# Kernel tuning notes

Hardware: AMD Instinct MI355X
Metric: run time of the kernel (lower is better)

## Reference

```python
import jax, jax.numpy as jnp
import numpy as np

NEG_BIG = -9e15
ALPHA = 0.2  # LeakyReLU negative slope


def setup_inputs() -> dict:
    key = jax.random.key(0)
    k1, k2, k3, k4 = jax.random.split(key, 4)
    N, Fin, Fout = 8192, 256, 256
    input_ = jax.random.normal(k1, (N, Fin), dtype=jnp.float32)
    adj = jax.random.randint(k2, (N, N), 0, 2, dtype=jnp.int32)
    # xavier_uniform with gain=1.414
    limW = 1.414 * np.sqrt(6.0 / (Fin + Fout))
    W = jax.random.uniform(k3, (Fin, Fout), minval=-limW, maxval=limW, dtype=jnp.float32)
    lima = 1.414 * np.sqrt(6.0 / (2 * Fout + 1))
    a = jax.random.uniform(k4, (2 * Fout, 1), minval=-lima, maxval=lima, dtype=jnp.float32)
    return {"input_": input_, "adj": adj, "W": W, "a": a}


def reference(input_, adj, W, a):
    # h: [N, F]
    h = input_ @ W
    F = h.shape[1]
    # Decompose cat([h_i, h_j]) @ a into per-node projections summed by broadcast
    src = h @ a[:F, 0]   # [N]  contribution of row node i
    dst = h @ a[F:, 0]   # [N]  contribution of col node j
    e = jax.nn.leaky_relu(src[:, None] + dst[None, :], negative_slope=ALPHA)  # [N, N]
    e = jnp.where(adj > 0, e, NEG_BIG)
    attention = jax.nn.softmax(e, axis=1)
    h_prime = attention @ h  # [N, F]
    return jax.nn.relu(h_prime)  # concat=True
```

## Files before the change

### kernel.cpp

```cpp
#include <hip/hip_runtime.h>
#include <math.h>

#define NN 8192
#define FF 256
#define ALPHA 0.2f
#define SS 4
#define JSEG (NN / SS)
#define STEPS (JSEG / 32)

typedef __bf16 bf16x8 __attribute__((ext_vector_type(8)));
typedef __bf16 bf16x4 __attribute__((ext_vector_type(4)));
typedef float  f32x4  __attribute__((ext_vector_type(4)));

__device__ __forceinline__ void dma16(const void* g, void* l) {
    __builtin_amdgcn_global_load_lds((const __attribute__((address_space(1))) void*)g,
                                     (__attribute__((address_space(3))) void*)l,
                                     16, 0, 0);
}

#define VMCNT0   asm volatile("s_waitcnt vmcnt(0)" ::: "memory")
#define LGKM0    asm volatile("s_waitcnt lgkmcnt(0)" ::: "memory")
#define BARRIER  asm volatile("s_barrier" ::: "memory")
#define FENCE    asm volatile("" ::: "memory")

__global__ __launch_bounds__(256) void k0_wt(const float* __restrict__ W,
                                             __bf16* __restrict__ WT) {
    __shared__ float ts[64][65];
    const int t = threadIdx.x;
    const int k0 = blockIdx.x * 64;
    const int n0 = blockIdx.y * 64;
    #pragma unroll
    for (int r = 0; r < 4; ++r) {
        int krow = r * 16 + (t >> 4);
        int nc4 = (t & 15) * 4;
        *(float4*)&ts[krow][nc4] = *(const float4*)&W[(size_t)(k0 + krow) * FF + n0 + nc4];
    }
    __syncthreads();
    const int nloc = t >> 2;
    const int kc = (t & 3) * 16;
    union { bf16x8 v[2]; __bf16 e[16]; } hi, lo;
    #pragma unroll
    for (int u = 0; u < 16; ++u) {
        float x = ts[kc + u][nloc];
        __bf16 h1 = (__bf16)x;
        hi.e[u] = h1;
        lo.e[u] = (__bf16)(x - (float)h1);
    }
    size_t base = (size_t)(n0 + nloc) * FF + k0 + kc;
    *(bf16x8*)&WT[base] = hi.v[0];
    *(bf16x8*)&WT[base + 8] = hi.v[1];
    size_t lbase = (size_t)FF * FF + base;
    *(bf16x8*)&WT[lbase] = lo.v[0];
    *(bf16x8*)&WT[lbase + 8] = lo.v[1];
}

__global__ __launch_bounds__(256) void k1_h(const float* __restrict__ X,
                                            const __bf16* __restrict__ WT,
                                            const float* __restrict__ a,
                                            __bf16* __restrict__ hT,
                                            float* __restrict__ src,
                                            float* __restrict__ dst) {
    __shared__ __bf16 ax[2][32][40];
    __shared__ float hs[32][264];
    __shared__ float red[2][4][32];
    const int t = threadIdx.x;
    const int i0 = blockIdx.x * 32;
    const int l = t & 63, wv = t >> 6, ln = l & 15, g = l >> 4;
    f32x4 acc[2][4];
    #pragma unroll
    for (int mt = 0; mt < 2; ++mt)
        #pragma unroll
        for (int nt = 0; nt < 4; ++nt)
            acc[mt][nt] = (f32x4){0.f, 0.f, 0.f, 0.f};

    for (int ks = 0; ks < 8; ++ks) {
        const int k0 = ks * 32;
        {
            int row = t >> 3, c4 = (t & 7) * 4;
            float4 xv = *(const float4*)&X[(size_t)(i0 + row) * FF + k0 + c4];
            bf16x4 hi4, lo4;
            float xs_[4] = {xv.x, xv.y, xv.z, xv.w};
            #pragma unroll
            for (int u = 0; u < 4; ++u) {
                __bf16 h1 = (__bf16)xs_[u];
                hi4[u] = h1;
                lo4[u] = (__bf16)(xs_[u] - (float)h1);
            }
            *(bf16x4*)&ax[0][row][c4] = hi4;
            *(bf16x4*)&ax[1][row][c4] = lo4;
        }
        __syncthreads();
        bf16x8 ah[2], al[2];
        ah[0] = *(bf16x8*)&ax[0][ln][g * 8];
        ah[1] = *(bf16x8*)&ax[0][16 + ln][g * 8];
        al[0] = *(bf16x8*)&ax[1][ln][g * 8];
        al[1] = *(bf16x8*)&ax[1][16 + ln][g * 8];
        #pragma unroll
        for (int nt = 0; nt < 4; ++nt) {
            const int n = wv * 64 + nt * 16 + ln;
            bf16x8 bh8 = *(const bf16x8*)&WT[(size_t)n * FF + k0 + g * 8];
            bf16x8 bl8 = *(const bf16x8*)&WT[(size_t)(FF + n) * FF + k0 + g * 8];
            #pragma unroll
            for (int mt = 0; mt < 2; ++mt) {
                acc[mt][nt] = __builtin_amdgcn_mfma_f32_16x16x32_bf16(ah[mt], bh8, acc[mt][nt], 0, 0, 0);
                acc[mt][nt] = __builtin_amdgcn_mfma_f32_16x16x32_bf16(ah[mt], bl8, acc[mt][nt], 0, 0, 0);
                acc[mt][nt] = __builtin_amdgcn_mfma_f32_16x16x32_bf16(al[mt], bh8, acc[mt][nt], 0, 0, 0);
            }
        }
        __syncthreads();
    }
    float an[4], ad[4];
    #pragma unroll
    for (int nt = 0; nt < 4; ++nt) {
        an[nt] = a[wv * 64 + nt * 16 + ln];
        ad[nt] = a[FF + wv * 64 + nt * 16 + ln];
    }
    float sp[2][4], dp[2][4];
    #pragma unroll
    for (int mt = 0; mt < 2; ++mt)
        #pragma unroll
        for (int rg = 0; rg < 4; ++rg) { sp[mt][rg] = 0.f; dp[mt][rg] = 0.f; }
    #pragma unroll
    for (int mt = 0; mt < 2; ++mt)
        #pragma unroll
        for (int nt = 0; nt < 4; ++nt)
            #pragma unroll
            for (int rg = 0; rg < 4; ++rg) {
                float v = acc[mt][nt][rg];
                hs[mt * 16 + g * 4 + rg][wv * 64 + nt * 16 + ln] = v;
                sp[mt][rg] += v * an[nt];
                dp[mt][rg] += v * ad[nt];
            }
    #pragma unroll
    for (int mk = 1; mk < 16; mk <<= 1)
        #pragma unroll
        for (int mt = 0; mt < 2; ++mt)
            #pragma unroll
            for (int rg = 0; rg < 4; ++rg) {
                sp[mt][rg] += __shfl_xor(sp[mt][rg], mk);
                dp[mt][rg] += __shfl_xor(dp[mt][rg], mk);
            }
    if (ln == 0) {
        #pragma unroll
        for (int mt = 0; mt < 2; ++mt)
            #pragma unroll
            for (int rg = 0; rg < 4; ++rg) {
                red[0][wv][mt * 16 + g * 4 + rg] = sp[mt][rg];
                red[1][wv][mt * 16 + g * 4 + rg] = dp[mt][rg];
            }
    }
    __syncthreads();
    if (t < 32) {
        src[i0 + t] = red[0][0][t] + red[0][1][t] + red[0][2][t] + red[0][3][t];
        dst[i0 + t] = red[1][0][t] + red[1][1][t] + red[1][2][t] + red[1][3][t];
    }
    {
        const int f = t;
        #pragma unroll
        for (int jc = 0; jc < 4; ++jc) {
            union { bf16x8 v; __bf16 e[8]; } hi;
            #pragma unroll
            for (int u = 0; u < 8; ++u) {
                float x = hs[jc * 8 + u][f];
                hi.e[u] = (__bf16)x;
            }
            *(bf16x8*)&hT[(size_t)f * NN + i0 + jc * 8] = hi.v;
        }
    }
}

__global__ __launch_bounds__(256) void k2a_pack(const int* __restrict__ adj,
                                                unsigned* __restrict__ bits) {
    const size_t total4 = (size_t)NN * NN / 4;
    const int l = threadIdx.x & 63;
    const int base = l & 56;
    size_t t = (size_t)blockIdx.x * 256 + threadIdx.x;
    const size_t stride = (size_t)gridDim.x * 256;
    for (; t < total4; t += stride) {
        int4 v = ((const int4*)adj)[t];
        unsigned nib = (unsigned)(v.x > 0) | ((unsigned)(v.y > 0) << 1)
                     | ((unsigned)(v.z > 0) << 2) | ((unsigned)(v.w > 0) << 3);
        unsigned w = 0;
        #pragma unroll
        for (int k = 0; k < 8; ++k)
            w |= (unsigned)__shfl((int)nib, base + k) << (4 * k);
        if ((l & 7) == 0)
            bits[t >> 3] = w;
    }
}

__global__ __launch_bounds__(256) void k2b_max(const float* __restrict__ dst,
                                               float* __restrict__ maxd) {
    __shared__ float red[256];
    float m = -1e30f;
    #pragma unroll
    for (int r = 0; r < NN / 1024; ++r) {
        float4 v = *(const float4*)&dst[(r * 256 + threadIdx.x) * 4];
        m = fmaxf(m, fmaxf(fmaxf(v.x, v.y), fmaxf(v.z, v.w)));
    }
    red[threadIdx.x] = m;
    __syncthreads();
    for (int s = 128; s > 0; s >>= 1) {
        if (threadIdx.x < s) red[threadIdx.x] = fmaxf(red[threadIdx.x], red[threadIdx.x + s]);
        __syncthreads();
    }
    if (threadIdx.x == 0) maxd[0] = red[0];
}

__global__ __launch_bounds__(256, 3) void k3_attn(const unsigned* __restrict__ bits,
                                                  const __bf16* __restrict__ hT,
                                                  const float* __restrict__ src,
                                                  const float* __restrict__ dst,
                                                  const float* __restrict__ maxd,
                                                  float* __restrict__ num,
                                                  float* __restrict__ den) {
    __shared__ __bf16 bh[2][1024 * 8];
    __shared__ unsigned mlds[64 * 68];
    __shared__ float dsts[JSEG];
    const int t = threadIdx.x;
    const int l = t & 63, wv = t >> 6, ln = l & 15, g = l >> 4;
    const int it = blockIdx.x & 127;
    const int seg = blockIdx.x >> 7;
    const int i0 = it * 64;
    const int jbeg = seg * JSEG;
    const int rl = wv * 16 + ln;
    const int row = i0 + rl;
    const float maxdv = maxd[0];
    const float src_r = src[row];
    const float e0 = src_r + maxdv;
    const float m_r = e0 > 0.f ? e0 : ALPHA * e0;

    {
        int r = t >> 2;
        const int4* gsrc = (const int4*)(bits + (size_t)(i0 + r) * (NN / 32) + (jbeg >> 5));
        int4* ldst = (int4*)&mlds[r * 68];
        #pragma unroll
        for (int u = 0; u < 4; ++u)
            ldst[u * 4 + (t & 3)] = gsrc[u * 4 + (t & 3)];
    }
    #pragma unroll
    for (int u = 0; u < 2; ++u)
        *(float4*)&dsts[(u * 256 + t) * 4] = *(const float4*)&dst[jbeg + (u * 256 + t) * 4];

    int ga[4], cb[4];
    #pragma unroll
    for (int r = 0; r < 4; ++r) {
        int cbase = r * 256 + wv * 64;
        int c = cbase + l;
        int f = c >> 2;
        int pc = c & 3;
        int jc = pc ^ ((f >> 1) & 3);
        ga[r] = f * NN + jc * 8;
        cb[r] = __builtin_amdgcn_readfirstlane(cbase);
    }
    const int rb = ln * 64 + ((g ^ ((ln >> 1) & 3)) * 16);
    const char* bh0 = (const char*)&bh[0][0] + rb;
    const char* bh1 = (const char*)&bh[1][0] + rb;

    #pragma unroll
    for (int r = 0; r < 4; ++r)
        dma16(&hT[ga[r] + jbeg], &bh[0][cb[r] * 8]);
    __syncthreads();

    float den_reg = 0.f;
    f32x4 acc[16];
    #pragma unroll
    for (int nt = 0; nt < 16; ++nt) acc[nt] = (f32x4){0.f, 0.f, 0.f, 0.f};

    for (int s = 0; s < STEPS; ++s) {
        unsigned mb = (mlds[rl * 68 + s] >> (g * 8)) & 0xffu;
        const float* dp = &dsts[s * 32 + g * 8];
        float4 dq0 = *(const float4*)dp;
        float4 dq1 = *(const float4*)(dp + 4);
        const float dv[8] = {dq0.x, dq0.y, dq0.z, dq0.w,
                             dq1.x, dq1.y, dq1.z, dq1.w};
        union { bf16x8 v; __bf16 e[8]; } af;
        #pragma unroll
        for (int u = 0; u < 8; ++u) {
            float e = src_r + dv[u];
            e = e > 0.f ? e : ALPHA * e;
            float ex = __expf(e - m_r);
            float w = (mb & (1u << u)) ? ex : 0.f;
            den_reg += w;
            af.e[u] = (__bf16)w;
        }
        FENCE; VMCNT0; LGKM0; BARRIER;
        {
            int sn = (s + 1 < STEPS) ? s + 1 : 0;
            int jn = jbeg + sn * 32;
            int p = (s + 1) & 1;
            #pragma unroll
            for (int r = 0; r < 4; ++r)
                dma16(&hT[ga[r] + jn], &bh[p][cb[r] * 8]);
        }
        FENCE;
        const char* bp = (s & 1) ? bh1 : bh0;
        #pragma unroll
        for (int nt = 0; nt < 16; ++nt) {
            bf16x8 bfr = *(const bf16x8*)(bp + nt * 1024);
            acc[nt] = __builtin_amdgcn_mfma_f32_16x16x32_bf16(af.v, bfr, acc[nt], 0, 0, 0);
        }
    }
    den_reg += __shfl_xor(den_reg, 16);
    den_reg += __shfl_xor(den_reg, 32);
    if (g == 0) den[(size_t)seg * NN + row] = den_reg;
    #pragma unroll
    for (int nt = 0; nt < 16; ++nt)
        #pragma unroll
        for (int rg = 0; rg < 4; ++rg)
            num[((size_t)seg * NN + i0 + wv * 16 + g * 4 + rg) * FF
                + nt * 16 + ln] = acc[nt][rg];
}

__global__ __launch_bounds__(256) void k4_out(const float* __restrict__ num,
                                              const float* __restrict__ den,
                                              float* __restrict__ out) {
    size_t f4 = (size_t)blockIdx.x * 256 + threadIdx.x;
    int i = (int)(f4 >> 6);
    int c4 = (int)(f4 & 63) << 2;
    float4 s = make_float4(0.f, 0.f, 0.f, 0.f);
    float d = 0.f;
    #pragma unroll
    for (int sg = 0; sg < SS; ++sg) {
        float4 v = *(const float4*)&num[((size_t)sg * NN + i) * FF + c4];
        s.x += v.x; s.y += v.y; s.z += v.z; s.w += v.w;
        d += den[(size_t)sg * NN + i];
    }
    float inv = 1.f / d;
    float4 o;
    o.x = fmaxf(s.x * inv, 0.f);
    o.y = fmaxf(s.y * inv, 0.f);
    o.z = fmaxf(s.z * inv, 0.f);
    o.w = fmaxf(s.w * inv, 0.f);
    *(float4*)&out[(size_t)i * FF + c4] = o;
}

extern "C" void kernel_launch(void* const* d_in, const int* in_sizes, int n_in,
                              void* d_out, int out_size, void* d_ws, size_t ws_size,
                              hipStream_t stream) {
    const float* X  = (const float*)d_in[0];
    const int*  adj = (const int*)d_in[1];
    const float* W  = (const float*)d_in[2];
    const float* a  = (const float*)d_in[3];
    float* out = (float*)d_out;
    char* ws = (char*)d_ws;

    const size_t off_hT   = 0;
    const size_t off_wt   = off_hT + (size_t)FF * NN * 2;
    const size_t off_src  = off_wt + (size_t)2 * FF * FF * 2;
    const size_t off_dst  = off_src + (size_t)NN * 4;
    const size_t off_maxd = off_dst + (size_t)NN * 4;
    const size_t off_num  = off_maxd + 256;
    const size_t off_den  = off_num + (size_t)SS * NN * FF * 4;
    const size_t off_bits = off_den + (size_t)SS * NN * 4;

    __bf16* hT_ws = (__bf16*)(ws + off_hT);
    __bf16* wt_ws = (__bf16*)(ws + off_wt);
    float* src_ws = (float*)(ws + off_src);
    float* dst_ws = (float*)(ws + off_dst);
    float* maxd   = (float*)(ws + off_maxd);
    float* num_ws = (float*)(ws + off_num);
    float* den_ws = (float*)(ws + off_den);
    unsigned* bits_ws = (unsigned*)(ws + off_bits);

    k2a_pack<<<2048, 256, 0, stream>>>(adj, bits_ws);
    k0_wt<<<dim3(FF / 64, FF / 64), 256, 0, stream>>>(W, wt_ws);
    k1_h<<<NN / 32, 256, 0, stream>>>(X, wt_ws, a, hT_ws, src_ws, dst_ws);
    k2b_max<<<1, 256, 0, stream>>>(dst_ws, maxd);
    k3_attn<<<(NN / 64) * SS, 256, 0, stream>>>(bits_ws, hT_ws, src_ws, dst_ws, maxd,
                                                num_ws, den_ws);
    k4_out<<<(NN * FF / 4) / 256, 256, 0, stream>>>(num_ws, den_ws, out);
}
```

Before: 456.2 us.

## Fuse adjacency bit-packing into attention kernel and triple-buffer hT DMA

Removes the separate adjacency packing kernel; each attention block now reads its int32 adjacency tile directly and packs it into LDS bitmasks via wave shuffles. The hT tile pipeline moves from double to triple buffering with a partial vmcnt wait so one DMA stays in flight across the barrier. This avoids a launch and the bits round-trip, but raises LDS use, drops occupancy target to 2 blocks per CU, and puts the adjacency load latency in the kernel prologue.

```diff
diff --git a/kernel.cpp b/kernel.cpp
--- a/kernel.cpp
+++ b/kernel.cpp
@@ -18,7 +18,7 @@
                                      16, 0, 0);
 }
 
-#define VMCNT0   asm volatile("s_waitcnt vmcnt(0)" ::: "memory")
+#define VMCNT4   asm volatile("s_waitcnt vmcnt(4)" ::: "memory")
 #define LGKM0    asm volatile("s_waitcnt lgkmcnt(0)" ::: "memory")
 #define BARRIER  asm volatile("s_barrier" ::: "memory")
 #define FENCE    asm volatile("" ::: "memory")
@@ -169,26 +169,6 @@
     }
 }
 
-__global__ __launch_bounds__(256) void k2a_pack(const int* __restrict__ adj,
-                                                unsigned* __restrict__ bits) {
-    const size_t total4 = (size_t)NN * NN / 4;
-    const int l = threadIdx.x & 63;
-    const int base = l & 56;
-    size_t t = (size_t)blockIdx.x * 256 + threadIdx.x;
-    const size_t stride = (size_t)gridDim.x * 256;
-    for (; t < total4; t += stride) {
-        int4 v = ((const int4*)adj)[t];
-        unsigned nib = (unsigned)(v.x > 0) | ((unsigned)(v.y > 0) << 1)
-                     | ((unsigned)(v.z > 0) << 2) | ((unsigned)(v.w > 0) << 3);
-        unsigned w = 0;
-        #pragma unroll
-        for (int k = 0; k < 8; ++k)
-            w |= (unsigned)__shfl((int)nib, base + k) << (4 * k);
-        if ((l & 7) == 0)
-            bits[t >> 3] = w;
-    }
-}
-
 __global__ __launch_bounds__(256) void k2b_max(const float* __restrict__ dst,
                                                float* __restrict__ maxd) {
     __shared__ float red[256];
@@ -207,14 +187,14 @@
     if (threadIdx.x == 0) maxd[0] = red[0];
 }
 
-__global__ __launch_bounds__(256, 3) void k3_attn(const unsigned* __restrict__ bits,
+__global__ __launch_bounds__(256, 2) void k3_attn(const int* __restrict__ adj,
                                                   const __bf16* __restrict__ hT,
                                                   const float* __restrict__ src,
                                                   const float* __restrict__ dst,
                                                   const float* __restrict__ maxd,
                                                   float* __restrict__ num,
                                                   float* __restrict__ den) {
-    __shared__ __bf16 bh[2][1024 * 8];
+    __shared__ __bf16 bh[3][1024 * 8];
     __shared__ unsigned mlds[64 * 68];
     __shared__ float dsts[JSEG];
     const int t = threadIdx.x;
@@ -230,18 +210,6 @@
     const float e0 = src_r + maxdv;
     const float m_r = e0 > 0.f ? e0 : ALPHA * e0;
 
-    {
-        int r = t >> 2;
-        const int4* gsrc = (const int4*)(bits + (size_t)(i0 + r) * (NN / 32) + (jbeg >> 5));
-        int4* ldst = (int4*)&mlds[r * 68];
-        #pragma unroll
-        for (int u = 0; u < 4; ++u)
-            ldst[u * 4 + (t & 3)] = gsrc[u * 4 + (t & 3)];
-    }
-    #pragma unroll
-    for (int u = 0; u < 2; ++u)
-        *(float4*)&dsts[(u * 256 + t) * 4] = *(const float4*)&dst[jbeg + (u * 256 + t) * 4];
-
     int ga[4], cb[4];
     #pragma unroll
     for (int r = 0; r < 4; ++r) {
@@ -254,19 +222,44 @@
         cb[r] = __builtin_amdgcn_readfirstlane(cbase);
     }
     const int rb = ln * 64 + ((g ^ ((ln >> 1) & 3)) * 16);
-    const char* bh0 = (const char*)&bh[0][0] + rb;
-    const char* bh1 = (const char*)&bh[1][0] + rb;
 
     #pragma unroll
     for (int r = 0; r < 4; ++r)
         dma16(&hT[ga[r] + jbeg], &bh[0][cb[r] * 8]);
+    FENCE;
+
+    {
+        const int sh = 4 * (t & 7);
+        #pragma unroll 4
+        for (int itp = 0; itp < 128; ++itp) {
+            int r = itp >> 1, p = itp & 1;
+            int4 v = *(const int4*)&adj[(size_t)(i0 + r) * NN + jbeg + p * 1024 + 4 * t];
+            unsigned x = ((unsigned)(v.x > 0) | ((unsigned)(v.y > 0) << 1)
+                        | ((unsigned)(v.z > 0) << 2) | ((unsigned)(v.w > 0) << 3)) << sh;
+            x |= __shfl_xor((int)x, 1);
+            x |= __shfl_xor((int)x, 2);
+            x |= __shfl_xor((int)x, 4);
+            if ((l & 7) == 0)
+                mlds[r * 68 + p * 32 + (t >> 3)] = x;
+        }
+    }
+    #pragma unroll
+    for (int u = 0; u < 2; ++u)
+        *(float4*)&dsts[(u * 256 + t) * 4] = *(const float4*)&dst[jbeg + (u * 256 + t) * 4];
+
     __syncthreads();
+
+    #pragma unroll
+    for (int r = 0; r < 4; ++r)
+        dma16(&hT[ga[r] + jbeg + 32], &bh[1][cb[r] * 8]);
+    FENCE;
 
     float den_reg = 0.f;
     f32x4 acc[16];
     #pragma unroll
     for (int nt = 0; nt < 16; ++nt) acc[nt] = (f32x4){0.f, 0.f, 0.f, 0.f};
 
+    int cur = 0;
     for (int s = 0; s < STEPS; ++s) {
         unsigned mb = (mlds[rl * 68 + s] >> (g * 8)) & 0xffu;
         const float* dp = &dsts[s * 32 + g * 8];
@@ -284,22 +277,25 @@
             den_reg += w;
             af.e[u] = (__bf16)w;
         }
-        FENCE; VMCNT0; LGKM0; BARRIER;
+        FENCE; VMCNT4; LGKM0; BARRIER;
         {
-            int sn = (s + 1 < STEPS) ? s + 1 : 0;
+            int sn = s + 2;
+            if (sn >= STEPS) sn -= STEPS;
             int jn = jbeg + sn * 32;
-            int p = (s + 1) & 1;
+            int dmb = cur + 2;
+            if (dmb >= 3) dmb -= 3;
             #pragma unroll
             for (int r = 0; r < 4; ++r)
-                dma16(&hT[ga[r] + jn], &bh[p][cb[r] * 8]);
+                dma16(&hT[ga[r] + jn], &bh[dmb][cb[r] * 8]);
         }
         FENCE;
-        const char* bp = (s & 1) ? bh1 : bh0;
+        const char* bp = (const char*)&bh[cur][0] + rb;
         #pragma unroll
         for (int nt = 0; nt < 16; ++nt) {
             bf16x8 bfr = *(const bf16x8*)(bp + nt * 1024);
             acc[nt] = __builtin_amdgcn_mfma_f32_16x16x32_bf16(af.v, bfr, acc[nt], 0, 0, 0);
         }
+        if (++cur == 3) cur = 0;
     }
     den_reg += __shfl_xor(den_reg, 16);
     den_reg += __shfl_xor(den_reg, 32);
@@ -352,7 +348,6 @@
     const size_t off_maxd = off_dst + (size_t)NN * 4;
     const size_t off_num  = off_maxd + 256;
     const size_t off_den  = off_num + (size_t)SS * NN * FF * 4;
-    const size_t off_bits = off_den + (size_t)SS * NN * 4;
 
     __bf16* hT_ws = (__bf16*)(ws + off_hT);
     __bf16* wt_ws = (__bf16*)(ws + off_wt);
@@ -361,13 +356,11 @@
     float* maxd   = (float*)(ws + off_maxd);
     float* num_ws = (float*)(ws + off_num);
     float* den_ws = (float*)(ws + off_den);
-    unsigned* bits_ws = (unsigned*)(ws + off_bits);
-
-    k2a_pack<<<2048, 256, 0, stream>>>(adj, bits_ws);
+
     k0_wt<<<dim3(FF / 64, FF / 64), 256, 0, stream>>>(W, wt_ws);
     k1_h<<<NN / 32, 256, 0, stream>>>(X, wt_ws, a, hT_ws, src_ws, dst_ws);
     k2b_max<<<1, 256, 0, stream>>>(dst_ws, maxd);
-    k3_attn<<<(NN / 64) * SS, 256, 0, stream>>>(bits_ws, hT_ws, src_ws, dst_ws, maxd,
+    k3_attn<<<(NN / 64) * SS, 256, 0, stream>>>(adj, hT_ws, src_ws, dst_ws, maxd,
                                                 num_ws, den_ws);
     k4_out<<<(NN * FF / 4) / 256, 256, 0, stream>>>(num_ws, den_ws, out);
 }
```

New measurement: 472.4 us. 3.6% more time.

## Replace LDS DMA with register-staged prefetch two steps ahead in attention kernel

Applied to the files above, without the earlier changes.

The attention kernel no longer uses global_load_lds DMA with an explicit vmcnt wait and barrier every step. It now loads hT tiles into registers two steps ahead, writes them into the alternate LDS buffer between MFMA phases, and unrolls the loop by two with one __syncthreads per half-step. Occupancy hint drops from 3 to 2 blocks per SIMD to make room for the extra staging registers. The aim is to hide global latency behind the weight computation and MFMAs, at the cost of more VGPRs, lower occupancy and explicit LDS stores.

```diff
diff --git a/kernel.cpp b/kernel.cpp
--- a/kernel.cpp
+++ b/kernel.cpp
@@ -11,17 +11,6 @@
 typedef __bf16 bf16x8 __attribute__((ext_vector_type(8)));
 typedef __bf16 bf16x4 __attribute__((ext_vector_type(4)));
 typedef float  f32x4  __attribute__((ext_vector_type(4)));
-
-__device__ __forceinline__ void dma16(const void* g, void* l) {
-    __builtin_amdgcn_global_load_lds((const __attribute__((address_space(1))) void*)g,
-                                     (__attribute__((address_space(3))) void*)l,
-                                     16, 0, 0);
-}
-
-#define VMCNT0   asm volatile("s_waitcnt vmcnt(0)" ::: "memory")
-#define LGKM0    asm volatile("s_waitcnt lgkmcnt(0)" ::: "memory")
-#define BARRIER  asm volatile("s_barrier" ::: "memory")
-#define FENCE    asm volatile("" ::: "memory")
 
 __global__ __launch_bounds__(256) void k0_wt(const float* __restrict__ W,
                                              __bf16* __restrict__ WT) {
@@ -207,7 +196,7 @@
     if (threadIdx.x == 0) maxd[0] = red[0];
 }
 
-__global__ __launch_bounds__(256, 3) void k3_attn(const unsigned* __restrict__ bits,
+__global__ __launch_bounds__(256, 2) void k3_attn(const unsigned* __restrict__ bits,
                                                   const __bf16* __restrict__ hT,
                                                   const float* __restrict__ src,
                                                   const float* __restrict__ dst,
@@ -230,6 +219,25 @@
     const float e0 = src_r + maxdv;
     const float m_r = e0 > 0.f ? e0 : ALPHA * e0;
 
+    int ga[4], lc[4];
+    #pragma unroll
+    for (int r = 0; r < 4; ++r) {
+        int c = r * 256 + wv * 64 + l;
+        int f = c >> 2;
+        int pc = c & 3;
+        int jc = pc ^ ((f >> 1) & 3);
+        ga[r] = f * NN + jc * 8;
+        lc[r] = c * 8;
+    }
+    const int rb = ln * 64 + ((g ^ ((ln >> 1) & 3)) * 16);
+    const char* bh0 = (const char*)&bh[0][0] + rb;
+    const char* bh1 = (const char*)&bh[1][0] + rb;
+
+    int4 rA[4], rB[4];
+    #pragma unroll
+    for (int r = 0; r < 4; ++r) rA[r] = *(const int4*)&hT[ga[r] + jbeg];
+    #pragma unroll
+    for (int r = 0; r < 4; ++r) rB[r] = *(const int4*)&hT[ga[r] + jbeg + 32];
     {
         int r = t >> 2;
         const int4* gsrc = (const int4*)(bits + (size_t)(i0 + r) * (NN / 32) + (jbeg >> 5));
@@ -241,25 +249,8 @@
     #pragma unroll
     for (int u = 0; u < 2; ++u)
         *(float4*)&dsts[(u * 256 + t) * 4] = *(const float4*)&dst[jbeg + (u * 256 + t) * 4];
-
-    int ga[4], cb[4];
-    #pragma unroll
-    for (int r = 0; r < 4; ++r) {
-        int cbase = r * 256 + wv * 64;
-        int c = cbase + l;
-        int f = c >> 2;
-        int pc = c & 3;
-        int jc = pc ^ ((f >> 1) & 3);
-        ga[r] = f * NN + jc * 8;
-        cb[r] = __builtin_amdgcn_readfirstlane(cbase);
-    }
-    const int rb = ln * 64 + ((g ^ ((ln >> 1) & 3)) * 16);
-    const char* bh0 = (const char*)&bh[0][0] + rb;
-    const char* bh1 = (const char*)&bh[1][0] + rb;
-
-    #pragma unroll
-    for (int r = 0; r < 4; ++r)
-        dma16(&hT[ga[r] + jbeg], &bh[0][cb[r] * 8]);
+    #pragma unroll
+    for (int r = 0; r < 4; ++r) *(int4*)&bh[0][lc[r]] = rA[r];
     __syncthreads();
 
     float den_reg = 0.f;
@@ -267,39 +258,60 @@
     #pragma unroll
     for (int nt = 0; nt < 16; ++nt) acc[nt] = (f32x4){0.f, 0.f, 0.f, 0.f};
 
-    for (int s = 0; s < STEPS; ++s) {
-        unsigned mb = (mlds[rl * 68 + s] >> (g * 8)) & 0xffu;
-        const float* dp = &dsts[s * 32 + g * 8];
-        float4 dq0 = *(const float4*)dp;
-        float4 dq1 = *(const float4*)(dp + 4);
-        const float dv[8] = {dq0.x, dq0.y, dq0.z, dq0.w,
-                             dq1.x, dq1.y, dq1.z, dq1.w};
-        union { bf16x8 v; __bf16 e[8]; } af;
-        #pragma unroll
-        for (int u = 0; u < 8; ++u) {
-            float e = src_r + dv[u];
-            e = e > 0.f ? e : ALPHA * e;
-            float ex = __expf(e - m_r);
-            float w = (mb & (1u << u)) ? ex : 0.f;
-            den_reg += w;
-            af.e[u] = (__bf16)w;
-        }
-        FENCE; VMCNT0; LGKM0; BARRIER;
-        {
-            int sn = (s + 1 < STEPS) ? s + 1 : 0;
-            int jn = jbeg + sn * 32;
-            int p = (s + 1) & 1;
+#define K3_WCOMP(S_, AF_)                                                     \
+    {                                                                         \
+        unsigned mb = (mlds[rl * 68 + (S_)] >> (g * 8)) & 0xffu;              \
+        const float* dp_ = &dsts[(S_) * 32 + g * 8];                          \
+        float4 dq0 = *(const float4*)dp_;                                     \
+        float4 dq1 = *(const float4*)(dp_ + 4);                               \
+        const float dv[8] = {dq0.x, dq0.y, dq0.z, dq0.w,                      \
+                             dq1.x, dq1.y, dq1.z, dq1.w};                     \
+        _Pragma("unroll")                                                     \
+        for (int u = 0; u < 8; ++u) {                                         \
+            float e = src_r + dv[u];                                          \
+            e = e > 0.f ? e : ALPHA * e;                                      \
+            float ex = __expf(e - m_r);                                       \
+            float w = (mb & (1u << u)) ? ex : 0.f;                            \
+            den_reg += w;                                                     \
+            AF_.e[u] = (__bf16)w;                                             \
+        }                                                                     \
+    }
+
+#define K3_MFMA(AF_, BP_)                                                     \
+    {                                                                         \
+        _Pragma("unroll")                                                     \
+        for (int nt = 0; nt < 16; ++nt) {                                     \
+            bf16x8 bfr = *(const bf16x8*)((BP_) + nt * 1024);                 \
+            acc[nt] = __builtin_amdgcn_mfma_f32_16x16x32_bf16(                \
+                AF_.v, bfr, acc[nt], 0, 0, 0);                                \
+        }                                                                     \
+    }
+
+    for (int s = 0; s < STEPS; s += 2) {
+        if (s + 2 < STEPS) {
             #pragma unroll
             for (int r = 0; r < 4; ++r)
-                dma16(&hT[ga[r] + jn], &bh[p][cb[r] * 8]);
-        }
-        FENCE;
-        const char* bp = (s & 1) ? bh1 : bh0;
-        #pragma unroll
-        for (int nt = 0; nt < 16; ++nt) {
-            bf16x8 bfr = *(const bf16x8*)(bp + nt * 1024);
-            acc[nt] = __builtin_amdgcn_mfma_f32_16x16x32_bf16(af.v, bfr, acc[nt], 0, 0, 0);
-        }
+                rA[r] = *(const int4*)&hT[ga[r] + jbeg + (s + 2) * 32];
+        }
+        union { bf16x8 v; __bf16 e[8]; } afe;
+        K3_WCOMP(s, afe);
+        #pragma unroll
+        for (int r = 0; r < 4; ++r) *(int4*)&bh[1][lc[r]] = rB[r];
+        K3_MFMA(afe, bh0);
+        __syncthreads();
+        if (s + 3 < STEPS) {
+            #pragma unroll
+            for (int r = 0; r < 4; ++r)
+                rB[r] = *(const int4*)&hT[ga[r] + jbeg + (s + 3) * 32];
+        }
+        union { bf16x8 v; __bf16 e[8]; } afo;
+        K3_WCOMP(s + 1, afo);
+        if (s + 2 < STEPS) {
+            #pragma unroll
+            for (int r = 0; r < 4; ++r) *(int4*)&bh[0][lc[r]] = rA[r];
+        }
+        K3_MFMA(afo, bh1);
+        __syncthreads();
     }
     den_reg += __shfl_xor(den_reg, 16);
     den_reg += __shfl_xor(den_reg, 32);
```

Measured after the change: 512.4 us. 1.12x slower.
